# Optimization experiments

Hardware: AMD Instinct MI355X
Metric: run time of the kernel (lower is better)

Reference implementation:

```python
import jax, jax.numpy as jnp
import numpy as np

B, T, WN = 256, 200, 200        # batch, char_num, word_num
H, CD, WD = 512, 30, 128        # hidden_dim, char_dim, word_dim
V, K = 128, 12                  # vocab, tag_size
START, STOP = 10, 11
HH = H // 2


def lstm_dir(x_tm, m_tm, Wih, Whh, b, reverse):
    # x_tm: [T,B,I], m_tm: [T,B,1] validity mask. Packed-sequence semantics:
    # state only updates on valid steps, padded outputs are zero. reverse=True
    # replicates the backward direction of a packed bidirectional LSTM.
    z = jnp.zeros((x_tm.shape[1], Whh.shape[1]), x_tm.dtype)
    def cell(carry, inp):
        h, c = carry
        xt, mt = inp
        g = xt @ Wih.T + h @ Whh.T + b              # [B,4H], gates i,f,g,o
        i, f, gc, o = jnp.split(g, 4, axis=-1)
        cn = jax.nn.sigmoid(f) * c + jax.nn.sigmoid(i) * jnp.tanh(gc)
        hn = jax.nn.sigmoid(o) * jnp.tanh(cn)
        return (jnp.where(mt, hn, h), jnp.where(mt, cn, c)), jnp.where(mt, hn, 0.0)
    _, ys = jax.lax.scan(cell, (z, z), (x_tm, m_tm), reverse=reverse)
    return ys


def bilstm(x, lens, Wih_f, Whh_f, b_f, Wih_b, Whh_b, b_b):
    Tn = x.shape[1]
    m = jnp.arange(Tn)[None, :] < lens[:, None]     # [B,T]
    x_tm = jnp.swapaxes(x, 0, 1)
    m_tm = m.T[:, :, None]
    hf = lstm_dir(x_tm, m_tm, Wih_f, Whh_f, b_f, False)
    hb = lstm_dir(x_tm, m_tm, Wih_b, Whh_b, b_b, True)
    return jnp.swapaxes(jnp.concatenate([hf, hb], -1), 0, 1)  # [B,T,H]


def encode(characters, words, len_char, len_word,
           char_emb, char_Wih_f, char_Whh_f, char_b_f, char_Wih_b, char_Whh_b, char_b_b,
           char_lin_W, char_lin_b,
           word_Wih_f, word_Whh_f, word_b_f, word_Wih_b, word_Whh_b, word_b_b,
           word_lin_W, word_lin_b, lin1_W, lin1_b, lin2_W, lin2_b, tag_W, tag_b):
    sp = jax.nn.softplus
    char_vec = char_emb[characters]                                   # [B,T,CD]
    char_h = bilstm(char_vec, len_char, char_Wih_f, char_Whh_f, char_b_f,
                    char_Wih_b, char_Whh_b, char_b_b)                 # [B,T,H]
    char_map = sp(char_h @ char_lin_W.T + char_lin_b)                 # [B,T,H]
    word_h = bilstm(words, len_word, word_Wih_f, word_Whh_f, word_b_f,
                    word_Wih_b, word_Whh_b, word_b_b)                 # [B,WN,H]
    word_map = sp(word_h @ word_lin_W.T + word_lin_b)                 # [B,WN,T]
    word_map = word_map.reshape(word_map.shape[0], T, -1)             # view, NOT transpose
    x = jnp.concatenate([char_map, word_map], axis=2)                 # [B,T,712]
    x = sp(x @ lin1_W.T + lin1_b)
    x = sp(x @ lin2_W.T + lin2_b)
    return sp(x @ tag_W.T + tag_b)                                    # [B,T,K]


def crf_nll(logits, tags, lens, trans):
    Bn, Tn, Kn = logits.shape
    mask = jnp.arange(Tn)[None, :] < lens[:, None]                    # [B,T]
    # --- real path score (transitions indexed [from, to], START prepended) ---
    prev = jnp.concatenate([jnp.full((Bn, 1), START, tags.dtype), tags[:, :-1]], axis=1)
    emit = jnp.take_along_axis(logits, tags[..., None], axis=-1)[..., 0]
    step = jnp.where(mask, emit + trans[prev, tags], 0.0)
    last_tag = jnp.take_along_axis(tags, (lens - 1)[:, None], axis=1)[:, 0]
    real = step.sum(axis=1) + trans[last_tag, STOP]
    # --- forward algorithm (alpha init 0, first step includes transitions, as in source) ---
    def fwd(alpha, inp):
        lt, m = inp                                                   # [B,K], [B]
        sc = alpha[:, :, None] + lt[:, None, :] + trans[None]         # [B,prev,next]
        an = jax.nn.logsumexp(sc, axis=1)
        return jnp.where(m[:, None], an, alpha), None
    alpha0 = jnp.zeros((Bn, Kn), logits.dtype)
    alpha, _ = jax.lax.scan(fwd, alpha0, (jnp.swapaxes(logits, 0, 1), mask.T))
    total = jax.nn.logsumexp(alpha + trans[:, STOP][None, :], axis=1)
    return (jnp.sum(total) - jnp.sum(real)).reshape(1)


def setup_inputs() -> dict:
    key = jax.random.key(0)
    ks = jax.random.split(key, 32)
    rn = lambda k, s: jax.random.normal(k, s, jnp.float32) * 0.1
    inp = {
        "characters": jax.random.randint(ks[0], (B, T), 0, V),
        "words": jax.random.normal(ks[1], (B, WN, WD), jnp.float32),
        "tags": jax.random.randint(ks[2], (B, T), 0, K - 2),
        "len_char": jax.random.randint(ks[3], (B,), 50, T + 1),
        "len_word": jax.random.randint(ks[4], (B,), 50, WN + 1),
        "char_emb": rn(ks[5], (V, CD)),
        "char_Wih_f": rn(ks[6], (4 * HH, CD)), "char_Whh_f": rn(ks[7], (4 * HH, HH)), "char_b_f": rn(ks[8], (4 * HH,)),
        "char_Wih_b": rn(ks[9], (4 * HH, CD)), "char_Whh_b": rn(ks[10], (4 * HH, HH)), "char_b_b": rn(ks[11], (4 * HH,)),
        "char_lin_W": rn(ks[12], (H, H)), "char_lin_b": rn(ks[13], (H,)),
        "word_Wih_f": rn(ks[14], (4 * HH, WD)), "word_Whh_f": rn(ks[15], (4 * HH, HH)), "word_b_f": rn(ks[16], (4 * HH,)),
        "word_Wih_b": rn(ks[17], (4 * HH, WD)), "word_Whh_b": rn(ks[18], (4 * HH, HH)), "word_b_b": rn(ks[19], (4 * HH,)),
        "word_lin_W": rn(ks[20], (T, H)), "word_lin_b": rn(ks[21], (T,)),
        "lin1_W": rn(ks[22], (512, H + WN)), "lin1_b": rn(ks[23], (512,)),
        "lin2_W": rn(ks[24], (256, 512)), "lin2_b": rn(ks[25], (256,)),
        "tag_W": rn(ks[26], (K, 256)), "tag_b": rn(ks[27], (K,)),
    }
    trans = jax.random.normal(ks[28], (K, K), jnp.float32)
    trans = trans.at[START, :].set(-10000.0).at[:, STOP].set(-10000.0)
    inp["transitions"] = trans
    return inp


def reference(characters, words, tags, len_char, len_word,
              char_emb, char_Wih_f, char_Whh_f, char_b_f, char_Wih_b, char_Whh_b, char_b_b,
              char_lin_W, char_lin_b,
              word_Wih_f, word_Whh_f, word_b_f, word_Wih_b, word_Whh_b, word_b_b,
              word_lin_W, word_lin_b, lin1_W, lin1_b, lin2_W, lin2_b, tag_W, tag_b, transitions):
    logits = encode(characters, words, len_char, len_word,
                    char_emb, char_Wih_f, char_Whh_f, char_b_f, char_Wih_b, char_Whh_b, char_b_b,
                    char_lin_W, char_lin_b,
                    word_Wih_f, word_Whh_f, word_b_f, word_Wih_b, word_Whh_b, word_b_b,
                    word_lin_W, word_lin_b, lin1_W, lin1_b, lin2_W, lin2_b, tag_W, tag_b)
    return crf_nll(logits, tags, len_char, transitions)
```

## Files before the change

### kernel.cpp

```cpp
#include <hip/hip_runtime.h>
#include <cstdint>

typedef __attribute__((ext_vector_type(8))) short short8;
typedef __attribute__((ext_vector_type(4))) float f32x4;
typedef __attribute__((ext_vector_type(2))) float f32x2;
typedef __attribute__((ext_vector_type(4))) int i32x4;
typedef unsigned short us16;
typedef unsigned char u8;

#define DEV __device__ __forceinline__

DEV u8 f2fp8(float f){
  int p = __builtin_amdgcn_cvt_pk_fp8_f32(f, f, 0, false);
  return (u8)(p & 0xFF);
}
template<int SEL> DEV float fp8tof(int dw){
#if __has_builtin(__builtin_amdgcn_cvt_f32_fp8)
  return __builtin_amdgcn_cvt_f32_fp8(dw, SEL);
#else
  int b = (dw >> (8*SEL)) & 255;
  int e = (b>>3)&15, m = b&7;
  float v;
  if (e){ union{unsigned u; float f;} x; x.u = (unsigned)(((e+120)<<23) | (m<<20)); v = x.f; }
  else v = (float)m * 0.001953125f;
  return (b & 128) ? -v : v;
#endif
}
DEV f32x4 dq8x4(int dw){
#if __has_builtin(__builtin_amdgcn_cvt_pk_f32_fp8)
  f32x2 lo = __builtin_amdgcn_cvt_pk_f32_fp8(dw, false);
  f32x2 hi = __builtin_amdgcn_cvt_pk_f32_fp8(dw, true);
  return (f32x4){lo.x, lo.y, hi.x, hi.y};
#else
  return (f32x4){fp8tof<0>(dw), fp8tof<1>(dw), fp8tof<2>(dw), fp8tof<3>(dw)};
#endif
}
DEV float fsig(float x){
  float e = __builtin_amdgcn_exp2f(-1.4426950408889634f * x);
  return __builtin_amdgcn_rcpf(1.0f + e);
}
DEV float ftanh(float x){
  float e = __builtin_amdgcn_exp2f(-2.8853900817779268f * x);
  return fmaf(2.0f, __builtin_amdgcn_rcpf(1.0f + e), -1.0f);
}
DEV float fsoftplus(float x){
  float ax = fabsf(x);
  float e = __builtin_amdgcn_exp2f(-1.4426950408889634f * ax);
  float l = 0.69314718055994531f * __builtin_amdgcn_logf(1.0f + e);
  return fmaxf(x, 0.0f) + l;
}
DEV f32x4 mfma16f8(long a, long b, f32x4 c){
  return __builtin_amdgcn_mfma_f32_16x16x32_fp8_fp8(a, b, c, 0, 0, 0);
}
DEV unsigned pk4fp8(float a, float b, float c, float d){
  unsigned lo = (unsigned)__builtin_amdgcn_cvt_pk_fp8_f32(a, b, 0, false) & 0xFFFFu;
  unsigned hi = (unsigned)__builtin_amdgcn_cvt_pk_fp8_f32(c, d, 0, false) & 0xFFFFu;
  return lo | (hi << 16);
}

DEV void lds_barrier(){
  asm volatile("s_waitcnt lgkmcnt(0)" ::: "memory");
  __builtin_amdgcn_s_barrier();
  asm volatile("" ::: "memory");
}



DEV void swz_lstm16_one(int tid, const float* __restrict__ W, u8* __restrict__ dst){
  int e = tid & 511, chunk = tid >> 9;
  int L = e >> 3, j = e & 7;
  int kc = chunk & 7, gt = (chunk >> 3) & 3, w = chunk >> 5;
  int g = gt * 256 + w * 16 + (L & 15);
  int k = kc * 32 + (L >> 4) * 8 + j;
  dst[tid] = f2fp8(W[g * 256 + k]);
}

DEV void ctab_one(int vd, int gcol, const float* __restrict__ emb,
                  const float* __restrict__ Wih, const float* __restrict__ bb,
                  u8* __restrict__ ctab){
  int v = vd & 127, dir = vd >> 7;
  float val[4];
  #pragma unroll
  for (int gt = 0; gt < 4; ++gt){
    int g = gt * 256 + gcol;
    float s = bb[g];
    for (int k = 0; k < 30; ++k) s += emb[v * 30 + k] * Wih[g * 30 + k];
    val[gt] = s;
  }
  unsigned pk = pk4fp8(val[0], val[1], val[2], val[3]);
  *(unsigned*)&ctab[((dir * 128 + v) * 256 + gcol) * 4] = pk;
}

DEV void swz_gin_one(int tid, const float* __restrict__ W, u8* __restrict__ dst){
  int e = tid & 511, chunk = tid >> 9;
  int L = e >> 3, j = e & 7;
  int kc = chunk & 3, ntile = chunk >> 2;
  int g = ntile * 16 + (L & 15);
  int k = kc * 32 + (L >> 4) * 8 + j;
  dst[tid] = f2fp8(W[g * 128 + k]);
}

DEV void swz_ffB_one(int tid, const float* W, int N, int Kd, int KCs, u8* dst){
  int e = tid & 511, chunk = tid >> 9;
  int L = e >> 3, j = e & 7;
  int kc = chunk % KCs; int nt = chunk / KCs;
  int g = nt * 16 + (L & 15);
  int k = kc * 32 + (L >> 4) * 8 + j;
  float v = (g < N && k < Kd) ? W[g * Kd + k] : 0.0f;
  dst[tid] = f2fp8(v);
}

DEV void swz_ffA_one(int tid, const float* W, int Kd, int KCs, u8* dst){
  int e = tid & 511, chunk = tid >> 9;
  int L = e >> 3, j = e & 7;
  int kc = chunk % KCs; int mt = chunk / KCs;
  int m = mt * 16 + (L & 15);
  int k = kc * 32 + (L >> 4) * 8 + j;
  float v = (k < Kd) ? W[m * Kd + k] : 0.0f;
  dst[tid] = f2fp8(v);
}

__global__ __launch_bounds__(256) void k_pre(
    const float* __restrict__ WhhA, u8* dA, const float* __restrict__ WhhB, u8* dB,
    const float* __restrict__ WhhC, u8* dC, const float* __restrict__ WhhD, u8* dD,
    const float* __restrict__ emb,
    const float* __restrict__ cWihF, const float* __restrict__ cbF,
    const float* __restrict__ cWihB, const float* __restrict__ cbB,
    u8* __restrict__ ctab,
    const float* __restrict__ gWf, const float* __restrict__ gWb,
    u8* __restrict__ dgf, u8* __restrict__ dgb,
    const float* __restrict__ W1, u8* d1, const float* __restrict__ W2, u8* d2,
    const float* __restrict__ W5, u8* d5,
    const float* __restrict__ W3, u8* d3, const float* __restrict__ W4, u8* d4)
{
  const int b = blockIdx.x, tid = threadIdx.x;
  if (b < 4096){
    if (b < 1024)       swz_lstm16_one(b * 256 + tid, WhhA, dA);
    else if (b < 2048)  swz_lstm16_one((b - 1024) * 256 + tid, WhhB, dB);
    else if (b < 3072)  swz_lstm16_one((b - 2048) * 256 + tid, WhhC, dC);
    else                swz_lstm16_one((b - 3072) * 256 + tid, WhhD, dD);
  } else if (b < 4352){
    int vd = b - 4096;
    ctab_one(vd, tid, emb, (vd >> 7) ? cWihB : cWihF, (vd >> 7) ? cbB : cbF, ctab);
  } else if (b < 5376){
    int bb = b - 4352;
    if (bb < 512) swz_gin_one(bb * 256 + tid, gWf, dgf);
    else          swz_gin_one((bb - 512) * 256 + tid, gWb, dgb);
  } else if (b < 6928){
    int bb = b - 5376;
    if (bb < 1024)      swz_ffB_one(bb * 256 + tid, W1, 512, 512, 16, d1);
    else if (bb < 1536) swz_ffB_one((bb - 1024) * 256 + tid, W2, 200, 512, 16, d2);
    else                swz_ffB_one((bb - 1536) * 256 + tid, W5, 12, 256, 8, d5);
  } else {
    int bb = b - 6928;
    if (bb < 1536) swz_ffA_one(bb * 256 + tid, W3, 712, 24, d3);
    else           swz_ffA_one((bb - 1536) * 256 + tid, W4, 512, 16, d4);
  }
}

__global__ __launch_bounds__(512) void k_gin(
    const float* __restrict__ words, const u8* __restrict__ wswg_f,
    const u8* __restrict__ wswg_b, const float* __restrict__ bias_f,
    const float* __restrict__ bias_b, u8* __restrict__ gin)
{
  const int blk = blockIdx.x;
  const int d = blk / 800, rem = blk - d * 800;
  const int slice = rem / 50, tq = rem - slice * 50;
  const u8* Wsw = d ? wswg_b : wswg_f;
  const float* bias = d ? bias_b : bias_f;
  __shared__ u8 xs[16 * 136];
  __shared__ u8 sbuf[4 * 4096];
  const int tid = threadIdx.x;
  const int wv = tid >> 6, L = tid & 63;
  const int lrow = L & 15, lq = L >> 4;
  const long* WswV = (const long*)Wsw;

  long wr[8][4];
  #pragma unroll
  for (int nt = 0; nt < 8; ++nt)
    #pragma unroll
    for (int kc = 0; kc < 4; ++kc)
      wr[nt][kc] = WswV[((wv * 8 + nt) * 4 + kc) * 64 + L];
  float bv[8];
  #pragma unroll
  for (int nt = 0; nt < 8; ++nt) bv[nt] = bias[wv * 128 + nt * 16 + lrow];

  for (int i = 0; i < 4; ++i){
    const int t = tq * 4 + i;
    {
      int r = tid >> 5, c4 = (tid & 31) * 4;
      f32x4 v = *(const f32x4*)&words[((long)(slice * 16 + r) * 200 + t) * 128 + c4];
      *(unsigned*)&xs[r * 136 + c4] = pk4fp8(v.x, v.y, v.z, v.w);
    }
    __syncthreads();
    f32x4 acc[8];
    #pragma unroll
    for (int nt = 0; nt < 8; ++nt) acc[nt] = (f32x4){bv[nt], bv[nt], bv[nt], bv[nt]};
    #pragma unroll
    for (int kc = 0; kc < 4; ++kc){
      long af = *(const long*)&xs[lrow * 136 + kc * 32 + lq * 8];
      #pragma unroll
      for (int nt = 0; nt < 8; ++nt)
        acc[nt] = mfma16f8(af, wr[nt][kc], acc[nt]);
    }
    #pragma unroll
    for (int nt = 0; nt < 8; ++nt){
      int c = wv * 128 + nt * 16 + lrow;
      int gt = c >> 8, hcol = c & 255;
      int base = (hcol >> 4) * 256 + (hcol & 15) * 4 + gt;
      #pragma unroll
      for (int r = 0; r < 4; ++r)
        sbuf[lq * 4096 + base + r * 64] = f2fp8(acc[nt][r]);
    }
    __syncthreads();
    #pragma unroll
    for (int q = 0; q < 4; ++q){
      long ob = ((long)((d * 64 + slice * 4 + q) * 200 + t)) * 4096 + tid * 8;
      *(long*)&gin[ob] = *(const long*)&sbuf[q * 4096 + tid * 8];
    }
    __syncthreads();
  }
}

template<bool CHARV>
DEV void lstm16_body(u8* abuf, u8* cidxs,
                     const u8* __restrict__ gsrc,
                     const int* __restrict__ chars,
                     const u8* __restrict__ Wsw,
                     const int* __restrict__ lens,
                     u8* __restrict__ hout,
                     int b0, int hcol0, bool rev, long ginBase)
{
  const int tid = threadIdx.x;
  const int w = tid >> 6, L = tid & 63;
  const int lrow = L & 15, lq = L >> 4;
  const int gcol = w * 16 + lrow;
  const long* WswV = (const long*)Wsw;

  long wr[4][8];
  #pragma unroll
  for (int gt = 0; gt < 4; ++gt)
    #pragma unroll
    for (int kc = 0; kc < 8; ++kc)
      wr[gt][kc] = WswV[(((w * 4 + gt) * 8) + kc) * 64 + L];

  const int mylen = lens[b0 + lq];
  const long hbase = (long)(b0 + lq) * 200 * 512 + hcol0 + gcol;

  float cst = 0.0f;
  u8 hst = 0, houtv = 0;

  for (int e = tid; e < 1120; e += 1024) ((long*)abuf)[e] = 0;

  if constexpr (CHARV){
    if (tid < 800) cidxs[tid] = (u8)chars[(b0 + tid / 200) * 200 + tid % 200];
  }
  __syncthreads();

  const int t0 = rev ? 199 : 0;
  unsigned gw;
  if constexpr (!CHARV)
    gw = *(const unsigned*)(gsrc + (ginBase + t0) * 4096 + tid * 4);
  else
    gw = *(const unsigned*)&gsrc[((int)cidxs[lq * 200 + t0] * 256 + gcol) * 4];

  for (int tau = 0; tau < 200; ++tau){
    const int t = rev ? (199 - tau) : tau;
    u8* cur = abuf + (tau & 1) * 4480;
    u8* nxt = abuf + ((tau & 1) ^ 1) * 4480;

    f32x4 q = dq8x4((int)gw);
    f32x4 acc[4];
    #pragma unroll
    for (int gt = 0; gt < 4; ++gt)
      acc[gt] = (f32x4){q[gt], q[gt], q[gt], q[gt]};

    {
      const int tn = (tau < 199) ? (rev ? t - 1 : t + 1) : t;
      if constexpr (!CHARV)
        gw = *(const unsigned*)(gsrc + (ginBase + tn) * 4096 + tid * 4);
      else
        gw = *(const unsigned*)&gsrc[((int)cidxs[lq * 200 + tn] * 256 + gcol) * 4];
    }

    #pragma unroll
    for (int kc = 0; kc < 8; ++kc){
      long af = *(const long*)&cur[lrow * 280 + kc * 32 + lq * 8];
      #pragma unroll
      for (int gt = 0; gt < 4; ++gt)
        acc[gt] = mfma16f8(af, wr[gt][kc], acc[gt]);
    }

    const bool mk = t < mylen;
    float gi = acc[0][0], gf = acc[1][0];
    float gg = acc[2][0], go = acc[3][0];
    float cn = fsig(gf) * cst + fsig(gi) * ftanh(gg);
    if (mk) cst = cn;
    float hn = fsig(go) * ftanh(cn);
    u8 p8 = f2fp8(hn);
    if (mk) hst = p8;
    houtv = mk ? p8 : (u8)0;
    nxt[(lq * 4) * 280 + gcol] = hst;
    hout[hbase + (long)t * 512] = houtv;

    lds_barrier();
  }
}

__global__ __launch_bounds__(1024) void k_lstm(
    const int* __restrict__ characters, const u8* __restrict__ gin,
    const u8* __restrict__ ctab,
    const u8* __restrict__ wsw_cf, const u8* __restrict__ wsw_cb,
    const u8* __restrict__ wsw_wf, const u8* __restrict__ wsw_wb,
    const int* __restrict__ len_char, const int* __restrict__ len_word,
    u8* __restrict__ h_char, u8* __restrict__ h_word)
{
  const int dir    = blockIdx.x >> 6;
  const int slice4 = blockIdx.x & 63;
  const int b0 = slice4 * 4;
  __shared__ __align__(16) u8 abuf[2 * 16 * 280];
  __shared__ u8 cidxs[4 * 200];

  if (dir == 0)
    lstm16_body<true>(abuf, cidxs, ctab, characters, wsw_cf,
                      len_char, h_char, b0, 0, false, 0);
  else if (dir == 1)
    lstm16_body<true>(abuf, cidxs, ctab + 131072, characters, wsw_cb,
                      len_char, h_char, b0, 256, true, 0);
  else if (dir == 2)
    lstm16_body<false>(abuf, cidxs, gin, nullptr, wsw_wf,
                       len_word, h_word, b0, 0, false, (long)slice4 * 200);
  else
    lstm16_body<false>(abuf, cidxs, gin, nullptr, wsw_wb,
                       len_word, h_word, b0, 256, true, (long)(64 + slice4) * 200);
}

DEV void g12_body(const u8* __restrict__ A, const u8* __restrict__ Wsw,
                  const float* __restrict__ bias, int N,
                  u8* __restrict__ outp, int ocol0, int m0base, int ntbase, u8* lds)
{
  const int tid = threadIdx.x;
  const int w = tid >> 6, L = tid & 63;
  const int lrow = L & 15, lq = L >> 4;
  const long* WswV = (const long*)Wsw;

  {
    const int row = tid >> 1, half = (tid & 1) * 256;
    #pragma unroll
    for (int q = 0; q < 16; ++q)
      *(i32x4*)&lds[row * 520 + half + q * 16] =
        *(const i32x4*)&A[(long)(m0base + row) * 512 + half + q * 16];
  }
  lds_barrier();

  f32x4 acc[8][2] = {};
  for (int kc = 0; kc < 16; ++kc){
    long af[2];
    #pragma unroll
    for (int m0 = 0; m0 < 2; ++m0)
      af[m0] = *(const long*)&lds[(w * 32 + m0 * 16 + lrow) * 520 + kc * 32 + lq * 8];
    #pragma unroll
    for (int nt = 0; nt < 8; ++nt){
      long bf = WswV[((ntbase + nt) * 16 + kc) * 64 + L];
      acc[nt][0] = mfma16f8(af[0], bf, acc[nt][0]);
      acc[nt][1] = mfma16f8(af[1], bf, acc[nt][1]);
    }
  }
  #pragma unroll
  for (int nt = 0; nt < 8; ++nt){
    const int col = (ntbase + nt) * 16 + lrow;
    const bool valid = col < N;
    const float bvv = valid ? bias[col] : 0.0f;
    #pragma unroll
    for (int m0 = 0; m0 < 2; ++m0){
      #pragma unroll
      for (int r = 0; r < 4; ++r){
        float v = fsoftplus(acc[nt][m0][r] + bvv);
        const long row = m0base + w * 32 + m0 * 16 + lq * 4 + r;
        outp[row * 768 + ocol0 + col] = valid ? f2fp8(v) : (u8)0;
      }
    }
  }
}

__global__ __launch_bounds__(256) void k_g12(
    const u8* __restrict__ hc, const u8* __restrict__ hw,
    const u8* __restrict__ w1, const u8* __restrict__ w2,
    const float* __restrict__ b1, const float* __restrict__ b2,
    u8* __restrict__ xcat)
{
  __shared__ __align__(16) u8 lds[128 * 520];
  const int y = blockIdx.y;
  if (y < 4)
    g12_body(hc, w1, b1, 512, xcat,   0, blockIdx.x * 128, y * 8, lds);
  else
    g12_body(hw, w2, b2, 200, xcat, 512, blockIdx.x * 128, (y - 4) * 8, lds);
}

__global__ __launch_bounds__(256) void k_tail(
    const u8* __restrict__ xcat, const u8* __restrict__ w3A,
    const u8* __restrict__ w4A, const u8* __restrict__ w5B,
    const float* __restrict__ b3, const float* __restrict__ b4,
    const float* __restrict__ b5, float* __restrict__ logits)
{
  __shared__ __align__(16) u8 sA[64 * 776];
  __shared__ __align__(16) u8 x1s[64 * 520];
  __shared__ __align__(16) u8 x2s[64 * 264];
  const int tid = threadIdx.x;
  const int w = tid >> 6, L = tid & 63;
  const int lrow = L & 15, lq = L >> 4;
  const int m0 = blockIdx.x * 64;
  const long* W3 = (const long*)w3A;
  const long* W4 = (const long*)w4A;
  const long* W5 = (const long*)w5B;

  {
    const int row = tid >> 2, seg = (tid & 3) * 192;
    #pragma unroll
    for (int q = 0; q < 12; ++q)
      *(i32x4*)&sA[row * 776 + seg + q * 16] =
        *(const i32x4*)&xcat[(long)(m0 + row) * 768 + seg + q * 16];
  }
  lds_barrier();

  f32x4 acc[8][4];
  #pragma unroll
  for (int mt = 0; mt < 8; ++mt)
    #pragma unroll
    for (int nt = 0; nt < 4; ++nt) acc[mt][nt] = (f32x4){0,0,0,0};

  for (int kc2 = 0; kc2 < 12; ++kc2){
    #pragma unroll
    for (int kk = 0; kk < 2; ++kk){
      long bf[4];
      #pragma unroll
      for (int nt = 0; nt < 4; ++nt)
        bf[nt] = *(const long*)&sA[(nt * 16 + lrow) * 776 + kc2 * 64 + kk * 32 + lq * 8];
      #pragma unroll
      for (int mt = 0; mt < 8; ++mt){
        long af = W3[((w * 8 + mt) * 24 + kc2 * 2 + kk) * 64 + L];
        #pragma unroll
        for (int nt = 0; nt < 4; ++nt)
          acc[mt][nt] = mfma16f8(af, bf[nt], acc[mt][nt]);
      }
    }
  }
  #pragma unroll
  for (int mt = 0; mt < 8; ++mt){
    const int ch0 = (w * 8 + mt) * 16 + lq * 4;
    f32x4 bb = *(const f32x4*)&b3[ch0];
    #pragma unroll
    for (int nt = 0; nt < 4; ++nt){
      const int bat = nt * 16 + lrow;
      unsigned pk = pk4fp8(fsoftplus(acc[mt][nt][0] + bb[0]),
                           fsoftplus(acc[mt][nt][1] + bb[1]),
                           fsoftplus(acc[mt][nt][2] + bb[2]),
                           fsoftplus(acc[mt][nt][3] + bb[3]));
      *(unsigned*)&x1s[bat * 520 + ch0] = pk;
    }
  }
  lds_barrier();

  f32x4 a2[4][4];
  #pragma unroll
  for (int mt = 0; mt < 4; ++mt)
    #pragma unroll
    for (int nt = 0; nt < 4; ++nt) a2[mt][nt] = (f32x4){0,0,0,0};
  for (int kc = 0; kc < 16; ++kc){
    long bf[4];
    #pragma unroll
    for (int nt = 0; nt < 4; ++nt)
      bf[nt] = *(const long*)&x1s[(nt * 16 + lrow) * 520 + kc * 32 + lq * 8];
    #pragma unroll
    for (int mt = 0; mt < 4; ++mt){
      long af = W4[((w * 4 + mt) * 16 + kc) * 64 + L];
      #pragma unroll
      for (int nt = 0; nt < 4; ++nt)
        a2[mt][nt] = mfma16f8(af, bf[nt], a2[mt][nt]);
    }
  }
  #pragma unroll
  for (int mt = 0; mt < 4; ++mt){
    const int ch0 = (w * 4 + mt) * 16 + lq * 4;
    f32x4 bb = *(const f32x4*)&b4[ch0];
    #pragma unroll
    for (int nt = 0; nt < 4; ++nt){
      const int bat = nt * 16 + lrow;
      unsigned pk = pk4fp8(fsoftplus(a2[mt][nt][0] + bb[0]),
                           fsoftplus(a2[mt][nt][1] + bb[1]),
                           fsoftplus(a2[mt][nt][2] + bb[2]),
                           fsoftplus(a2[mt][nt][3] + bb[3]));
      *(unsigned*)&x2s[bat * 264 + ch0] = pk;
    }
  }
  lds_barrier();

  f32x4 a3 = (f32x4){0,0,0,0};
  #pragma unroll
  for (int kc = 0; kc < 8; ++kc){
    long af = *(const long*)&x2s[(w * 16 + lrow) * 264 + kc * 32 + lq * 8];
    long bf = W5[kc * 64 + L];
    a3 = mfma16f8(af, bf, a3);
  }
  if (lrow < 12){
    float bb = b5[lrow];
    #pragma unroll
    for (int r = 0; r < 4; ++r)
      logits[(long)(m0 + w * 16 + lq * 4 + r) * 12 + lrow] = fsoftplus(a3[r] + bb);
  }
}

__global__ void k_crf(const float* __restrict__ logits, const int* __restrict__ tags,
                      const int* __restrict__ lens, const float* __restrict__ trans,
                      float* __restrict__ nll)
{
  const int b = blockIdx.x;
  const int lane = threadIdx.x;
  __shared__ float sl[2400];
  for (int e = lane; e < 2400; e += 64) sl[e] = logits[(long)b * 2400 + e];
  const int lj = (lane < 12) ? lane : 0;
  float tcol[12];
  #pragma unroll
  for (int i = 0; i < 12; ++i) tcol[i] = trans[i * 12 + lj];
  const int len = lens[b];
  float alpha = 0.0f;
  __syncthreads();

  for (int t = 0; t < len; ++t){
    float av[12];
    #pragma unroll
    for (int i = 0; i < 12; ++i)
      av[i] = __shfl(alpha, i, 64) + tcol[i];
    float mx = av[0];
    #pragma unroll
    for (int i = 1; i < 12; ++i) mx = fmaxf(mx, av[i]);
    float ss = 0.0f;
    #pragma unroll
    for (int i = 0; i < 12; ++i)
      ss += __builtin_amdgcn_exp2f(1.4426950408889634f * (av[i] - mx));
    alpha = sl[t * 12 + lj] + mx + 0.69314718055994531f * __builtin_amdgcn_logf(ss);
  }

  float tv = alpha + trans[lj * 12 + 11];
  float tmax = tv;
  #pragma unroll
  for (int i = 0; i < 12; ++i) tmax = fmaxf(tmax, __shfl(tv, i, 64));
  float tss = 0.0f;
  #pragma unroll
  for (int i = 0; i < 12; ++i)
    tss += __builtin_amdgcn_exp2f(1.4426950408889634f * (__shfl(tv, i, 64) - tmax));

  float rs = 0.0f;
  for (int t = lane; t < len; t += 64){
    int tg = tags[b * 200 + t];
    int pv = (t == 0) ? 10 : tags[b * 200 + t - 1];
    rs += sl[t * 12 + tg] + trans[pv * 12 + tg];
  }
  #pragma unroll
  for (int off = 32; off > 0; off >>= 1) rs += __shfl_down(rs, off, 64);
  if (lane == 0){
    float total = tmax + 0.69314718055994531f * __builtin_amdgcn_logf(tss);
    rs += trans[tags[b * 200 + len - 1] * 12 + 11];
    nll[b] = total - rs;
  }
}

__global__ void k_sum(const float* __restrict__ nll, float* __restrict__ out){
  __shared__ float red[256];
  int t = threadIdx.x;
  red[t] = nll[t];
  __syncthreads();
  for (int s = 128; s > 0; s >>= 1){
    if (t < s) red[t] += red[t + s];
    __syncthreads();
  }
  if (t == 0) out[0] = red[0];
}

extern "C" void kernel_launch(void* const* d_in, const int* in_sizes, int n_in,
                              void* d_out, int out_size, void* d_ws, size_t ws_size,
                              hipStream_t stream)
{
  (void)in_sizes; (void)n_in; (void)out_size; (void)ws_size;
  const int*   characters = (const int*)  d_in[0];
  const float* words      = (const float*)d_in[1];
  const int*   tags       = (const int*)  d_in[2];
  const int*   len_char   = (const int*)  d_in[3];
  const int*   len_word   = (const int*)  d_in[4];
  const float* char_emb   = (const float*)d_in[5];
  const float* char_Wih_f = (const float*)d_in[6];
  const float* char_Whh_f = (const float*)d_in[7];
  const float* char_b_f   = (const float*)d_in[8];
  const float* char_Wih_b = (const float*)d_in[9];
  const float* char_Whh_b = (const float*)d_in[10];
  const float* char_b_b   = (const float*)d_in[11];
  const float* char_lin_W = (const float*)d_in[12];
  const float* char_lin_b = (const float*)d_in[13];
  const float* word_Wih_f = (const float*)d_in[14];
  const float* word_Whh_f = (const float*)d_in[15];
  const float* word_b_f   = (const float*)d_in[16];
  const float* word_Wih_b = (const float*)d_in[17];
  const float* word_Whh_b = (const float*)d_in[18];
  const float* word_b_b   = (const float*)d_in[19];
  const float* word_lin_W = (const float*)d_in[20];
  const float* word_lin_b = (const float*)d_in[21];
  const float* lin1_W     = (const float*)d_in[22];
  const float* lin1_b     = (const float*)d_in[23];
  const float* lin2_W     = (const float*)d_in[24];
  const float* lin2_b     = (const float*)d_in[25];
  const float* tag_W      = (const float*)d_in[26];
  const float* tag_b      = (const float*)d_in[27];
  const float* trans      = (const float*)d_in[28];

  char* ws = (char*)d_ws;
  size_t off = 0;
  auto take = [&](size_t bytes) -> char* {
    char* p = ws + off;
    off = (off + bytes + 511) & ~(size_t)511;
    return p;
  };
  u8*   wsw_cf   = (u8*)take((size_t)262144);
  u8*   wsw_cb   = (u8*)take((size_t)262144);
  u8*   wsw_wf   = (u8*)take((size_t)262144);
  u8*   wsw_wb   = (u8*)take((size_t)262144);
  u8*   ctab     = (u8*)take((size_t)262144);
  u8*   wswgin_f = (u8*)take((size_t)64*4*512);
  u8*   wswgin_b = (u8*)take((size_t)64*4*512);
  u8*   wswg1    = (u8*)take((size_t)32*16*512);
  u8*   wswg2    = (u8*)take((size_t)16*16*512);
  u8*   wswg3    = (u8*)take((size_t)32*24*512);
  u8*   wswg4    = (u8*)take((size_t)16*16*512);
  u8*   wswg5    = (u8*)take((size_t)1*8*512);
  float* logits  = (float*)take((size_t)51200*12*4);
  float* nll     = (float*)take((size_t)256*4);
  u8*   h_char   = (u8*)take((size_t)51200*512);
  u8*   h_word   = (u8*)take((size_t)51200*512);
  u8*   gin      = (u8*)take((size_t)105*1024*1024);
  u8*   x_cat    = gin;

  k_pre<<<8976, 256, 0, stream>>>(
      char_Whh_f, wsw_cf, char_Whh_b, wsw_cb, word_Whh_f, wsw_wf, word_Whh_b, wsw_wb,
      char_emb, char_Wih_f, char_b_f, char_Wih_b, char_b_b, ctab,
      word_Wih_f, word_Wih_b, wswgin_f, wswgin_b,
      char_lin_W, wswg1, word_lin_W, wswg2, tag_W, wswg5,
      lin1_W, wswg3, lin2_W, wswg4);

  k_gin<<<1600, 512, 0, stream>>>(words, wswgin_f, wswgin_b, word_b_f, word_b_b, gin);

  k_lstm<<<256, 1024, 0, stream>>>(characters, gin, ctab,
                                   wsw_cf, wsw_cb, wsw_wf, wsw_wb,
                                   len_char, len_word, h_char, h_word);

  k_g12<<<dim3(400, 6), 256, 0, stream>>>(h_char, h_word, wswg1, wswg2,
                                          char_lin_b, word_lin_b, x_cat);
  k_tail<<<800, 256, 0, stream>>>(x_cat, wswg3, wswg4, wswg5,
                                  lin1_b, lin2_b, tag_b, logits);

  k_crf<<<256, 64, 0, stream>>>(logits, tags, len_char, trans, nll);
  k_sum<<<1, 256, 0, stream>>>(nll, (float*)d_out);
}
```

Before: 677.6 us.

## Stream A tiles through small LDS buffer with register prefetch in g12 and tail GEMMs

Replaces the up-front full-row LDS staging in k_g12 and k_tail with a K-chunked loop. Each iteration stages a 64-byte slice in a small LDS tile and prefetches the next slice into registers while MFMAs run. This shrinks LDS use, so occupancy can rise (k_tail now requests 2 blocks per CU) and the global load latency is hidden behind compute. In exchange it adds two barriers per chunk and makes the LDS reads and writes finer-grained.

```diff
diff --git a/kernel.cpp b/kernel.cpp
--- a/kernel.cpp
+++ b/kernel.cpp
@@ -343,28 +343,38 @@
   const int w = tid >> 6, L = tid & 63;
   const int lrow = L & 15, lq = L >> 4;
   const long* WswV = (const long*)Wsw;
-
-  {
-    const int row = tid >> 1, half = (tid & 1) * 256;
-    #pragma unroll
-    for (int q = 0; q < 16; ++q)
-      *(i32x4*)&lds[row * 520 + half + q * 16] =
-        *(const i32x4*)&A[(long)(m0base + row) * 512 + half + q * 16];
-  }
-  lds_barrier();
-
   f32x4 acc[8][2] = {};
-  for (int kc = 0; kc < 16; ++kc){
-    long af[2];
+  const int srow = tid >> 1, scol = (tid & 1) * 32;
+
+  i32x4 v0 = *(const i32x4*)&A[(long)(m0base + srow) * 512 + scol];
+  i32x4 v1 = *(const i32x4*)&A[(long)(m0base + srow) * 512 + scol + 16];
+
+  for (int kc2 = 0; kc2 < 8; ++kc2){
+    *(long*)&lds[srow * 72 + scol]      = ((const long*)&v0)[0];
+    *(long*)&lds[srow * 72 + scol + 8]  = ((const long*)&v0)[1];
+    *(long*)&lds[srow * 72 + scol + 16] = ((const long*)&v1)[0];
+    *(long*)&lds[srow * 72 + scol + 24] = ((const long*)&v1)[1];
+    lds_barrier();
+    if (kc2 < 7){
+      const long ab = (long)(m0base + srow) * 512 + (kc2 + 1) * 64 + scol;
+      v0 = *(const i32x4*)&A[ab];
+      v1 = *(const i32x4*)&A[ab + 16];
+    }
+    long af[2][2];
     #pragma unroll
     for (int m0 = 0; m0 < 2; ++m0)
-      af[m0] = *(const long*)&lds[(w * 32 + m0 * 16 + lrow) * 520 + kc * 32 + lq * 8];
-    #pragma unroll
-    for (int nt = 0; nt < 8; ++nt){
-      long bf = WswV[((ntbase + nt) * 16 + kc) * 64 + L];
-      acc[nt][0] = mfma16f8(af[0], bf, acc[nt][0]);
-      acc[nt][1] = mfma16f8(af[1], bf, acc[nt][1]);
-    }
+      #pragma unroll
+      for (int kk = 0; kk < 2; ++kk)
+        af[m0][kk] = *(const long*)&lds[(w * 32 + m0 * 16 + lrow) * 72 + kk * 32 + lq * 8];
+    #pragma unroll
+    for (int kk = 0; kk < 2; ++kk)
+      #pragma unroll
+      for (int nt = 0; nt < 8; ++nt){
+        long bf = WswV[((ntbase + nt) * 16 + kc2 * 2 + kk) * 64 + L];
+        acc[nt][0] = mfma16f8(af[0][kk], bf, acc[nt][0]);
+        acc[nt][1] = mfma16f8(af[1][kk], bf, acc[nt][1]);
+      }
+    lds_barrier();
   }
   #pragma unroll
   for (int nt = 0; nt < 8; ++nt){
@@ -389,7 +399,7 @@
     const float* __restrict__ b1, const float* __restrict__ b2,
     u8* __restrict__ xcat)
 {
-  __shared__ __align__(16) u8 lds[128 * 520];
+  __shared__ __align__(16) u8 lds[128 * 72];
   const int y = blockIdx.y;
   if (y < 4)
     g12_body(hc, w1, b1, 512, xcat,   0, blockIdx.x * 128, y * 8, lds);
@@ -397,13 +407,13 @@
     g12_body(hw, w2, b2, 200, xcat, 512, blockIdx.x * 128, (y - 4) * 8, lds);
 }
 
-__global__ __launch_bounds__(256) void k_tail(
+__global__ __launch_bounds__(256, 2) void k_tail(
     const u8* __restrict__ xcat, const u8* __restrict__ w3A,
     const u8* __restrict__ w4A, const u8* __restrict__ w5B,
     const float* __restrict__ b3, const float* __restrict__ b4,
     const float* __restrict__ b5, float* __restrict__ logits)
 {
-  __shared__ __align__(16) u8 sA[64 * 776];
+  __shared__ __align__(16) u8 sA[64 * 72];
   __shared__ __align__(16) u8 x1s[64 * 520];
   __shared__ __align__(16) u8 x2s[64 * 264];
   const int tid = threadIdx.x;
@@ -414,28 +424,26 @@
   const long* W4 = (const long*)w4A;
   const long* W5 = (const long*)w5B;
 
-  {
-    const int row = tid >> 2, seg = (tid & 3) * 192;
-    #pragma unroll
-    for (int q = 0; q < 12; ++q)
-      *(i32x4*)&sA[row * 776 + seg + q * 16] =
-        *(const i32x4*)&xcat[(long)(m0 + row) * 768 + seg + q * 16];
-  }
-  lds_barrier();
-
   f32x4 acc[8][4];
   #pragma unroll
   for (int mt = 0; mt < 8; ++mt)
     #pragma unroll
     for (int nt = 0; nt < 4; ++nt) acc[mt][nt] = (f32x4){0,0,0,0};
-
+  const int srow = tid >> 2, sc = (tid & 3) * 16;
+
+  i32x4 v = *(const i32x4*)&xcat[(long)(m0 + srow) * 768 + sc];
   for (int kc2 = 0; kc2 < 12; ++kc2){
+    *(long*)&sA[srow * 72 + sc]     = ((const long*)&v)[0];
+    *(long*)&sA[srow * 72 + sc + 8] = ((const long*)&v)[1];
+    lds_barrier();
+    if (kc2 < 11)
+      v = *(const i32x4*)&xcat[(long)(m0 + srow) * 768 + (kc2 + 1) * 64 + sc];
     #pragma unroll
     for (int kk = 0; kk < 2; ++kk){
       long bf[4];
       #pragma unroll
       for (int nt = 0; nt < 4; ++nt)
-        bf[nt] = *(const long*)&sA[(nt * 16 + lrow) * 776 + kc2 * 64 + kk * 32 + lq * 8];
+        bf[nt] = *(const long*)&sA[(nt * 16 + lrow) * 72 + kk * 32 + lq * 8];
       #pragma unroll
       for (int mt = 0; mt < 8; ++mt){
         long af = W3[((w * 8 + mt) * 24 + kc2 * 2 + kk) * 64 + L];
@@ -444,6 +452,7 @@
           acc[mt][nt] = mfma16f8(af, bf[nt], acc[mt][nt]);
       }
     }
+    lds_barrier();
   }
   #pragma unroll
   for (int mt = 0; mt < 8; ++mt){
```

Measured after the change: 646.8 us, median of 2. 1.05x faster.
